# Optimization experiments

Hardware: AMD Instinct MI355X
Metric: run time of the kernel (lower is better)

## Reference

```python
import jax, jax.numpy as jnp
import numpy as np

N, D, H2, E = 4096, 1024, 4096, 8  # tokens, input_dim, 2*hidden_dim, num_experts
H = H2 // 2


def setup_inputs() -> dict:
    key = jax.random.key(0)
    k1, k2, k3 = jax.random.split(key, 3)
    x = jax.random.normal(k1, (N, D), dtype=jnp.float32)
    expert_weights = jax.random.normal(k2, (E, D, H2), dtype=jnp.float32) * (1.0 / np.sqrt(D))
    expert_indices = jax.random.randint(k3, (N,), 0, E, dtype=jnp.int32)
    return {"x": x, "expert_weights": expert_weights, "expert_indices": expert_indices}


def reference(x, expert_weights, expert_indices):
    # Grouped GEMM equivalent: each token n is processed by expert e = expert_indices[n]:
    #   h_n = x_n @ W_e            -> [2H]
    #   out_n = silu(h[:H]) * h[H:] (SwiGLU)
    # jit-friendly dense-dispatch: project with all experts, then gather the assigned one.
    h_all = jnp.einsum('nd,edh->neh', x, expert_weights)            # [N, E, 2H]
    h = jnp.take_along_axis(h_all, expert_indices[:, None, None].astype(jnp.int32), axis=1)[:, 0]  # [N, 2H]
    a, b = h[:, :H], h[:, H:]
    return jax.nn.silu(a) * b                                        # [N, H]
```

## Files before the change

kernel.cpp:

```cpp
#include <hip/hip_runtime.h>
#include <hip/hip_bf16.h>

#define N_TOK 4096
#define DIM   1024
#define H2V   4096
#define HV    2048
#define NE    8
#define BM    256
#define BN    128
#define BK    64
#define NTHR  512
#define KSTEPS (DIM / BK)
#define CT_TILES (HV / BN)
#define RT_SLOTS (N_TOK / BM)
#define NPAIR (NE * CT_TILES)

#define WS_COUNTS 0
#define WS_BASE   64
#define WS_SLOTS  128
#define WS_XPERM  66560

typedef __attribute__((ext_vector_type(4))) float  f32x4;
typedef __attribute__((ext_vector_type(8))) short  s16x8;

__device__ __forceinline__ unsigned short f2bf(float f) {
    union { __hip_bfloat16 h; unsigned short u; } v;
    v.h = __float2bfloat16(f);
    return v.u;
}

__global__ void k_init(int* __restrict__ counts) {
    if (threadIdx.x < NE) counts[threadIdx.x] = 0;
}

__global__ void k_scatter(const int* __restrict__ idx, int* __restrict__ counts,
                          unsigned short* __restrict__ slots) {
    int n = blockIdx.x * blockDim.x + threadIdx.x;
    if (n < N_TOK) {
        int e = idx[n];
        int p = atomicAdd(&counts[e], 1);
        slots[e * N_TOK + p] = (unsigned short)n;
    }
}

__global__ void k_base(const int* __restrict__ counts, int* __restrict__ base) {
    if (threadIdx.x == 0) {
        int b = 0;
#pragma unroll
        for (int e = 0; e < NE; ++e) { base[e] = b; b += counts[e]; }
        base[NE] = b;
    }
}

__global__ void k_gather(const float* __restrict__ X, const int* __restrict__ base,
                         const unsigned short* __restrict__ slots,
                         unsigned short* __restrict__ Xp) {
    const int r    = blockIdx.x * 4 + (threadIdx.x >> 6);
    const int lane = threadIdx.x & 63;
    int e = 0;
#pragma unroll
    for (int i = 0; i < NE - 1; ++i) if (r >= base[i + 1]) e = i + 1;
    const int tok = slots[e * N_TOK + (r - base[e])];
    const float* src = X + (size_t)tok * DIM + lane * 16;
    unsigned short* dst = Xp + (size_t)r * DIM + lane * 16;
    f32x4 v0 = *(const f32x4*)(src);
    f32x4 v1 = *(const f32x4*)(src + 4);
    f32x4 v2 = *(const f32x4*)(src + 8);
    f32x4 v3 = *(const f32x4*)(src + 12);
    unsigned short t0[8], t1[8];
#pragma unroll
    for (int i = 0; i < 4; ++i) { t0[i] = f2bf(v0[i]); t0[4 + i] = f2bf(v1[i]); }
#pragma unroll
    for (int i = 0; i < 4; ++i) { t1[i] = f2bf(v2[i]); t1[4 + i] = f2bf(v3[i]); }
    *(s16x8*)(dst)     = *(const s16x8*)t0;
    *(s16x8*)(dst + 8) = *(const s16x8*)t1;
}

__global__ __launch_bounds__(NTHR, 2) void k_gemm(
        const float* __restrict__ W, const int* __restrict__ counts,
        const int* __restrict__ base, const unsigned short* __restrict__ slots,
        const unsigned short* __restrict__ Xp, float* __restrict__ out) {
    const int bid = blockIdx.x;
    const int p   = bid & (NPAIR - 1);
    const int rt  = bid >> 7;
    const int e   = p >> 4;
    const int ct  = p & (CT_TILES - 1);
    const int cnt = counts[e];
    const int tbase = rt * BM;
    if (tbase >= cnt) return;

    __shared__ unsigned short As[BM * BK];
    __shared__ unsigned short Bs[2 * BN * BK];

    const int t    = threadIdx.x;
    const int lane = t & 63;
    const int wid  = t >> 6;
    const int wm   = wid >> 1;
    const int wn   = wid & 1;
    const int l16  = lane & 15;
    const int g16  = lane >> 4;

    const unsigned short* aptr[4];
#pragma unroll
    for (int j = 0; j < 4; ++j) {
        int i  = wid * 4 + j;
        int rl = i * 8 + (lane >> 3);
        int qs = (lane & 7) ^ ((lane >> 3) & 7);
        int slot = tbase + rl;
        aptr[j] = Xp + (size_t)(base[e] + min(slot, cnt - 1)) * DIM + qs * 8;
    }
    const int c0 = (t & 31) * 4 + ((t >> 8) & 1) * 128;
    const int ko = (t >> 5) & 7;
    const int gcol = ct * BN + (c0 & 127) + (c0 >> 7) * HV;
    const float* bptr = W + (size_t)e * DIM * H2V + (size_t)(ko * 8) * H2V + gcol;

    f32x4 acc[2][4][4];
    const f32x4 zero = {0.f, 0.f, 0.f, 0.f};
#pragma unroll
    for (int g = 0; g < 2; ++g)
#pragma unroll
        for (int m = 0; m < 4; ++m)
#pragma unroll
            for (int n = 0; n < 4; ++n) acc[g][m][n] = zero;

    f32x4 bv[8];

    auto issueA = [&](int ks) {
#pragma unroll
        for (int j = 0; j < 4; ++j) {
            const unsigned short* g = aptr[j] + ks * BK;
            unsigned short* l = (unsigned short*)&As[(wid * 4 + j) * 512];
            __builtin_amdgcn_global_load_lds(
                (const __attribute__((address_space(1))) unsigned int*)(const void*)g,
                (__attribute__((address_space(3))) unsigned int*)(void*)l, 16, 0, 0);
        }
    };
    auto loadB = [&](int ks) {
#pragma unroll
        for (int i = 0; i < 8; ++i)
            bv[i] = *(const f32x4*)(bptr + (size_t)(ks * BK + i) * H2V);
    };
    auto storeB = [&]() {
#pragma unroll
        for (int j = 0; j < 4; ++j) {
            int c = c0 + j;
            int key = ((c >> 1) ^ (c >> 4)) & 7;
            unsigned short tmp[8];
#pragma unroll
            for (int i = 0; i < 8; ++i) tmp[i] = f2bf(bv[i][j]);
            *(s16x8*)&Bs[c * 64 + ((ko ^ key) * 8)] = *(const s16x8*)tmp;
        }
    };
    auto mfmaPhase = [&]() {
        __builtin_amdgcn_s_setprio(1);
#pragma unroll
        for (int kk = 0; kk < 2; ++kk) {
            const int gran = kk * 4 + g16;
            s16x8 af[4], bfr[2][4];
#pragma unroll
            for (int m = 0; m < 4; ++m) {
                int row = wm * 64 + m * 16 + l16;
                af[m] = *(const s16x8*)&As[row * 64 + ((gran ^ (row & 7)) * 8)];
            }
#pragma unroll
            for (int g = 0; g < 2; ++g)
#pragma unroll
                for (int n = 0; n < 4; ++n) {
                    int c = g * 128 + wn * 64 + n * 16 + l16;
                    int key = ((c >> 1) ^ (c >> 4)) & 7;
                    bfr[g][n] = *(const s16x8*)&Bs[c * 64 + ((gran ^ key) * 8)];
                }
#pragma unroll
            for (int g = 0; g < 2; ++g)
#pragma unroll
                for (int m = 0; m < 4; ++m)
#pragma unroll
                    for (int n = 0; n < 4; ++n)
                        acc[g][m][n] = __builtin_amdgcn_mfma_f32_16x16x32_bf16(
                            af[m], bfr[g][n], acc[g][m][n], 0, 0, 0);
        }
        __builtin_amdgcn_s_setprio(0);
    };

    issueA(0);
    loadB(0);
    asm volatile("s_waitcnt vmcnt(0)" ::: "memory");
    __builtin_amdgcn_sched_barrier(0);
    storeB();
    loadB(1);
    asm volatile("s_waitcnt lgkmcnt(0)" ::: "memory");
    __builtin_amdgcn_sched_barrier(0);
    __builtin_amdgcn_s_barrier();

#pragma unroll 1
    for (int ks = 0; ks < KSTEPS; ++ks) {
        mfmaPhase();
        if (ks + 1 < KSTEPS) {
            __builtin_amdgcn_s_barrier();
            issueA(ks + 1);
            asm volatile("s_waitcnt vmcnt(4)" ::: "memory");
            __builtin_amdgcn_sched_barrier(0);
            storeB();
            if (ks + 2 < KSTEPS) {
                loadB(ks + 2);
                asm volatile("s_waitcnt vmcnt(8) lgkmcnt(0)" ::: "memory");
            } else {
                asm volatile("s_waitcnt vmcnt(0) lgkmcnt(0)" ::: "memory");
            }
            __builtin_amdgcn_sched_barrier(0);
            __builtin_amdgcn_s_barrier();
        }
    }

    const unsigned short* ids = slots + e * N_TOK;
#pragma unroll
    for (int m = 0; m < 4; ++m) {
#pragma unroll
        for (int r = 0; r < 4; ++r) {
            int rowt = wm * 64 + m * 16 + g16 * 4 + r;
            int slot = tbase + rowt;
            if (slot < cnt) {
                int tok = ids[slot];
#pragma unroll
                for (int n = 0; n < 4; ++n) {
                    int col = ct * BN + wn * 64 + n * 16 + l16;
                    float a = acc[0][m][n][r];
                    float b = acc[1][m][n][r];
                    float sg = a / (1.0f + __expf(-a));
                    out[(size_t)tok * HV + col] = sg * b;
                }
            }
        }
    }
}

extern "C" void kernel_launch(void* const* d_in, const int* in_sizes, int n_in,
                              void* d_out, int out_size, void* d_ws, size_t ws_size,
                              hipStream_t stream) {
    const float* X  = (const float*)d_in[0];
    const float* W  = (const float*)d_in[1];
    const int* idx  = (const int*)d_in[2];
    float* out      = (float*)d_out;

    int* counts = (int*)((char*)d_ws + WS_COUNTS);
    int* base   = (int*)((char*)d_ws + WS_BASE);
    unsigned short* slots = (unsigned short*)((char*)d_ws + WS_SLOTS);
    unsigned short* Xp    = (unsigned short*)((char*)d_ws + WS_XPERM);

    k_init<<<1, 64, 0, stream>>>(counts);
    k_scatter<<<N_TOK / 256, 256, 0, stream>>>(idx, counts, slots);
    k_base<<<1, 64, 0, stream>>>(counts, base);
    k_gather<<<N_TOK / 4, 256, 0, stream>>>(X, base, slots, Xp);
    k_gemm<<<RT_SLOTS * NPAIR, NTHR, 0, stream>>>(W, counts, base, slots, Xp, out);
}
```

Baseline: 111.6 us.

## Double-buffer GEMM LDS tiles and interleave fragment reads with MFMA phases

Measured after the change: 122.5 us. 9.8% more time.

```diff
diff --git a/kernel.cpp b/kernel.cpp
--- a/kernel.cpp
+++ b/kernel.cpp
@@ -89,8 +89,8 @@
     const int tbase = rt * BM;
     if (tbase >= cnt) return;
 
-    __shared__ unsigned short As[BM * BK];
-    __shared__ unsigned short Bs[2 * BN * BK];
+    __shared__ unsigned short As[2][BM * BK];
+    __shared__ unsigned short Bs[2][2 * BN * BK];
 
     const int t    = threadIdx.x;
     const int lane = t & 63;
@@ -124,12 +124,13 @@
             for (int n = 0; n < 4; ++n) acc[g][m][n] = zero;
 
     f32x4 bv[8];
-
-    auto issueA = [&](int ks) {
+    s16x8 af0[2], af1[2], bfr[2][4];
+
+    auto issueA = [&](int ks, int buf) {
 #pragma unroll
         for (int j = 0; j < 4; ++j) {
             const unsigned short* g = aptr[j] + ks * BK;
-            unsigned short* l = (unsigned short*)&As[(wid * 4 + j) * 512];
+            unsigned short* l = (unsigned short*)&As[buf][(wid * 4 + j) * 512];
             __builtin_amdgcn_global_load_lds(
                 (const __attribute__((address_space(1))) unsigned int*)(const void*)g,
                 (__attribute__((address_space(3))) unsigned int*)(void*)l, 16, 0, 0);
@@ -140,7 +141,7 @@
         for (int i = 0; i < 8; ++i)
             bv[i] = *(const f32x4*)(bptr + (size_t)(ks * BK + i) * H2V);
     };
-    auto storeB = [&]() {
+    auto storeB = [&](int buf) {
 #pragma unroll
         for (int j = 0; j < 4; ++j) {
             int c = c0 + j;
@@ -148,68 +149,91 @@
             unsigned short tmp[8];
 #pragma unroll
             for (int i = 0; i < 8; ++i) tmp[i] = f2bf(bv[i][j]);
-            *(s16x8*)&Bs[c * 64 + ((ko ^ key) * 8)] = *(const s16x8*)tmp;
-        }
-    };
-    auto mfmaPhase = [&]() {
+            *(s16x8*)&Bs[buf][c * 64 + ((ko ^ key) * 8)] = *(const s16x8*)tmp;
+        }
+    };
+    auto dsAF = [&](s16x8 (&af)[2], int cur, int kk, int mh) {
+        const int gran = kk * 4 + g16;
+#pragma unroll
+        for (int mi = 0; mi < 2; ++mi) {
+            int row = wm * 64 + (mh * 2 + mi) * 16 + l16;
+            af[mi] = *(const s16x8*)&As[cur][row * 64 + ((gran ^ (row & 7)) * 8)];
+        }
+    };
+    auto dsBFR = [&](int cur, int kk) {
+        const int gran = kk * 4 + g16;
+#pragma unroll
+        for (int g = 0; g < 2; ++g)
+#pragma unroll
+            for (int n = 0; n < 4; ++n) {
+                int c = g * 128 + wn * 64 + n * 16 + l16;
+                int key = ((c >> 1) ^ (c >> 4)) & 7;
+                bfr[g][n] = *(const s16x8*)&Bs[cur][c * 64 + ((gran ^ key) * 8)];
+            }
+    };
+    auto mfma16 = [&](const s16x8 (&af)[2], int mh) {
         __builtin_amdgcn_s_setprio(1);
 #pragma unroll
-        for (int kk = 0; kk < 2; ++kk) {
-            const int gran = kk * 4 + g16;
-            s16x8 af[4], bfr[2][4];
-#pragma unroll
-            for (int m = 0; m < 4; ++m) {
-                int row = wm * 64 + m * 16 + l16;
-                af[m] = *(const s16x8*)&As[row * 64 + ((gran ^ (row & 7)) * 8)];
-            }
-#pragma unroll
-            for (int g = 0; g < 2; ++g)
-#pragma unroll
-                for (int n = 0; n < 4; ++n) {
-                    int c = g * 128 + wn * 64 + n * 16 + l16;
-                    int key = ((c >> 1) ^ (c >> 4)) & 7;
-                    bfr[g][n] = *(const s16x8*)&Bs[c * 64 + ((gran ^ key) * 8)];
-                }
-#pragma unroll
-            for (int g = 0; g < 2; ++g)
-#pragma unroll
-                for (int m = 0; m < 4; ++m)
-#pragma unroll
-                    for (int n = 0; n < 4; ++n)
-                        acc[g][m][n] = __builtin_amdgcn_mfma_f32_16x16x32_bf16(
-                            af[m], bfr[g][n], acc[g][m][n], 0, 0, 0);
-        }
+        for (int g = 0; g < 2; ++g)
+#pragma unroll
+            for (int mi = 0; mi < 2; ++mi)
+#pragma unroll
+                for (int n = 0; n < 4; ++n)
+                    acc[g][mh * 2 + mi][n] = __builtin_amdgcn_mfma_f32_16x16x32_bf16(
+                        af[mi], bfr[g][n], acc[g][mh * 2 + mi][n], 0, 0, 0);
         __builtin_amdgcn_s_setprio(0);
     };
-
-    issueA(0);
+#define LGKM0_SB  do { asm volatile("s_waitcnt lgkmcnt(0)" ::: "memory"); \
+                       __builtin_amdgcn_sched_barrier(0); } while (0)
+
+    issueA(0, 0);
     loadB(0);
     asm volatile("s_waitcnt vmcnt(0)" ::: "memory");
     __builtin_amdgcn_sched_barrier(0);
-    storeB();
+    storeB(0);
     loadB(1);
     asm volatile("s_waitcnt lgkmcnt(0)" ::: "memory");
     __builtin_amdgcn_sched_barrier(0);
     __builtin_amdgcn_s_barrier();
 
 #pragma unroll 1
-    for (int ks = 0; ks < KSTEPS; ++ks) {
-        mfmaPhase();
-        if (ks + 1 < KSTEPS) {
-            __builtin_amdgcn_s_barrier();
-            issueA(ks + 1);
+    for (int k = 0; k < KSTEPS; ++k) {
+        const int cur = k & 1;
+        dsAF(af0, cur, 0, 0);
+        dsBFR(cur, 0);
+        if (k + 1 < KSTEPS) issueA(k + 1, cur ^ 1);
+        __builtin_amdgcn_s_barrier();
+        LGKM0_SB;
+        mfma16(af0, 0);
+        __builtin_amdgcn_s_barrier();
+        dsAF(af1, cur, 0, 1);
+        __builtin_amdgcn_s_barrier();
+        LGKM0_SB;
+        mfma16(af1, 1);
+        __builtin_amdgcn_s_barrier();
+        dsAF(af0, cur, 1, 0);
+        dsBFR(cur, 1);
+        __builtin_amdgcn_s_barrier();
+        LGKM0_SB;
+        mfma16(af0, 0);
+        __builtin_amdgcn_s_barrier();
+        dsAF(af1, cur, 1, 1);
+        if (k + 1 < KSTEPS) {
             asm volatile("s_waitcnt vmcnt(4)" ::: "memory");
             __builtin_amdgcn_sched_barrier(0);
-            storeB();
-            if (ks + 2 < KSTEPS) {
-                loadB(ks + 2);
-                asm volatile("s_waitcnt vmcnt(8) lgkmcnt(0)" ::: "memory");
+            storeB(cur ^ 1);
+            if (k + 2 < KSTEPS) {
+                loadB(k + 2);
+                asm volatile("s_waitcnt vmcnt(8)" ::: "memory");
             } else {
-                asm volatile("s_waitcnt vmcnt(0) lgkmcnt(0)" ::: "memory");
+                asm volatile("s_waitcnt vmcnt(0)" ::: "memory");
             }
             __builtin_amdgcn_sched_barrier(0);
-            __builtin_amdgcn_s_barrier();
-        }
+        }
+        __builtin_amdgcn_s_barrier();
+        LGKM0_SB;
+        mfma16(af1, 1);
+        __builtin_amdgcn_s_barrier();
     }
 
     const unsigned short* ids = slots + e * N_TOK;
@@ -232,6 +256,7 @@
             }
         }
     }
+#undef LGKM0_SB
 }
 
 extern "C" void kernel_launch(void* const* d_in, const int* in_sizes, int n_in,
```

## Double-buffer LDS tiles to overlap next-step loads with MFMA compute

Applied to the files above, without the earlier changes.

Measured after the change: 115.2 us. 3.3% more time.

```diff
diff --git a/kernel.cpp b/kernel.cpp
--- a/kernel.cpp
+++ b/kernel.cpp
@@ -89,8 +89,8 @@
     const int tbase = rt * BM;
     if (tbase >= cnt) return;
 
-    __shared__ unsigned short As[BM * BK];
-    __shared__ unsigned short Bs[2 * BN * BK];
+    __shared__ unsigned short As[2][BM * BK];
+    __shared__ unsigned short Bs[2][2 * BN * BK];
 
     const int t    = threadIdx.x;
     const int lane = t & 63;
@@ -125,11 +125,11 @@
 
     f32x4 bv[8];
 
-    auto issueA = [&](int ks) {
+    auto issueA = [&](int ks, int buf) {
 #pragma unroll
         for (int j = 0; j < 4; ++j) {
             const unsigned short* g = aptr[j] + ks * BK;
-            unsigned short* l = (unsigned short*)&As[(wid * 4 + j) * 512];
+            unsigned short* l = (unsigned short*)&As[buf][(wid * 4 + j) * 512];
             __builtin_amdgcn_global_load_lds(
                 (const __attribute__((address_space(1))) unsigned int*)(const void*)g,
                 (__attribute__((address_space(3))) unsigned int*)(void*)l, 16, 0, 0);
@@ -140,7 +140,7 @@
         for (int i = 0; i < 8; ++i)
             bv[i] = *(const f32x4*)(bptr + (size_t)(ks * BK + i) * H2V);
     };
-    auto storeB = [&]() {
+    auto storeB = [&](int buf) {
 #pragma unroll
         for (int j = 0; j < 4; ++j) {
             int c = c0 + j;
@@ -148,11 +148,10 @@
             unsigned short tmp[8];
 #pragma unroll
             for (int i = 0; i < 8; ++i) tmp[i] = f2bf(bv[i][j]);
-            *(s16x8*)&Bs[c * 64 + ((ko ^ key) * 8)] = *(const s16x8*)tmp;
-        }
-    };
-    auto mfmaPhase = [&]() {
-        __builtin_amdgcn_s_setprio(1);
+            *(s16x8*)&Bs[buf][c * 64 + ((ko ^ key) * 8)] = *(const s16x8*)tmp;
+        }
+    };
+    auto mfmaPhase = [&](int cur) {
 #pragma unroll
         for (int kk = 0; kk < 2; ++kk) {
             const int gran = kk * 4 + g16;
@@ -160,7 +159,7 @@
 #pragma unroll
             for (int m = 0; m < 4; ++m) {
                 int row = wm * 64 + m * 16 + l16;
-                af[m] = *(const s16x8*)&As[row * 64 + ((gran ^ (row & 7)) * 8)];
+                af[m] = *(const s16x8*)&As[cur][row * 64 + ((gran ^ (row & 7)) * 8)];
             }
 #pragma unroll
             for (int g = 0; g < 2; ++g)
@@ -168,7 +167,7 @@
                 for (int n = 0; n < 4; ++n) {
                     int c = g * 128 + wn * 64 + n * 16 + l16;
                     int key = ((c >> 1) ^ (c >> 4)) & 7;
-                    bfr[g][n] = *(const s16x8*)&Bs[c * 64 + ((gran ^ key) * 8)];
+                    bfr[g][n] = *(const s16x8*)&Bs[cur][c * 64 + ((gran ^ key) * 8)];
                 }
 #pragma unroll
             for (int g = 0; g < 2; ++g)
@@ -179,34 +178,37 @@
                         acc[g][m][n] = __builtin_amdgcn_mfma_f32_16x16x32_bf16(
                             af[m], bfr[g][n], acc[g][m][n], 0, 0, 0);
         }
-        __builtin_amdgcn_s_setprio(0);
-    };
-
-    issueA(0);
+    };
+
+    issueA(0, 0);
     loadB(0);
     asm volatile("s_waitcnt vmcnt(0)" ::: "memory");
     __builtin_amdgcn_sched_barrier(0);
-    storeB();
+    storeB(0);
     loadB(1);
     asm volatile("s_waitcnt lgkmcnt(0)" ::: "memory");
     __builtin_amdgcn_sched_barrier(0);
     __builtin_amdgcn_s_barrier();
 
 #pragma unroll 1
-    for (int ks = 0; ks < KSTEPS; ++ks) {
-        mfmaPhase();
-        if (ks + 1 < KSTEPS) {
-            __builtin_amdgcn_s_barrier();
-            issueA(ks + 1);
+    for (int k = 0; k < KSTEPS; ++k) {
+        const int cur = k & 1;
+        if (k + 1 < KSTEPS) {
+            issueA(k + 1, cur ^ 1);
             asm volatile("s_waitcnt vmcnt(4)" ::: "memory");
             __builtin_amdgcn_sched_barrier(0);
-            storeB();
-            if (ks + 2 < KSTEPS) {
-                loadB(ks + 2);
-                asm volatile("s_waitcnt vmcnt(8) lgkmcnt(0)" ::: "memory");
+            storeB(cur ^ 1);
+            if (k + 2 < KSTEPS) loadB(k + 2);
+        }
+        mfmaPhase(cur);
+        if (k + 1 < KSTEPS) {
+            if (k + 2 < KSTEPS) {
+                asm volatile("s_waitcnt vmcnt(8)" ::: "memory");
             } else {
-                asm volatile("s_waitcnt vmcnt(0) lgkmcnt(0)" ::: "memory");
+                asm volatile("s_waitcnt vmcnt(0)" ::: "memory");
             }
+            __builtin_amdgcn_sched_barrier(0);
+            asm volatile("s_waitcnt lgkmcnt(0)" ::: "memory");
             __builtin_amdgcn_sched_barrier(0);
             __builtin_amdgcn_s_barrier();
         }
```
